# Kernel optimization log

Measured on AMD Instinct MI355X. Metric: run time of the kernel, lower is better.

The kernel has to match this reference:

```python
import jax, jax.numpy as jnp
import numpy as np

B, T, C = 2, 2048, 2048
N_HEAD, KV_HEADS = 16, 4
HEAD_DIM = C // N_HEAD  # 128
EPS = 1e-6


def setup_inputs() -> dict:
    key = jax.random.key(0)
    ks = jax.random.split(key, 3)
    x = jax.random.normal(ks[0], (B, T, C), dtype=jnp.float32)
    qkv_out = (N_HEAD + 2 * KV_HEADS) * HEAD_DIM  # 3072
    w_qkv = jax.random.normal(ks[1], (qkv_out, C), dtype=jnp.float32) * 0.02
    w_proj = jax.random.normal(ks[2], (C, C), dtype=jnp.float32) * 0.02
    q_norm_w = jnp.ones((HEAD_DIM,), dtype=jnp.float32)
    k_norm_w = jnp.ones((HEAD_DIM,), dtype=jnp.float32)
    # RoPE frequencies: theta = 10000^{-2i/d}, angles = pos * theta
    inv_freq = 1.0 / (10000.0 ** (np.arange(0, HEAD_DIM, 2, dtype=np.float32) / HEAD_DIM))
    angles = np.arange(T, dtype=np.float32)[:, None] * inv_freq[None, :]  # [T, 64]
    freqs_cos = jnp.asarray(np.cos(angles), dtype=jnp.float32)
    freqs_sin = jnp.asarray(np.sin(angles), dtype=jnp.float32)
    return {"x": x, "w_qkv": w_qkv, "w_proj": w_proj,
            "q_norm_w": q_norm_w, "k_norm_w": k_norm_w,
            "freqs_cos": freqs_cos, "freqs_sin": freqs_sin}


def _rope(t, cos, sin):
    # t: [B, H, T, D]; interpret last dim as D/2 complex pairs (a, b)
    a = t[..., 0::2]
    b = t[..., 1::2]
    oa = a * cos - b * sin
    ob = a * sin + b * cos
    return jnp.stack([oa, ob], axis=-1).reshape(t.shape)


def _rmsnorm(t, w, eps=EPS):
    rms = jnp.sqrt(jnp.mean(t * t, axis=-1, keepdims=True) + eps)
    return w * (t / rms)


def reference(x, w_qkv, w_proj, q_norm_w, k_norm_w, freqs_cos, freqs_sin):
    b, t, c = x.shape
    hd = HEAD_DIM
    qkv = x @ w_qkv.T  # [B, T, 3072]
    q_size = N_HEAD * hd
    kv_size = KV_HEADS * hd
    q = qkv[..., :q_size].reshape(b, t, N_HEAD, hd).transpose(0, 2, 1, 3)
    k = qkv[..., q_size:q_size + kv_size].reshape(b, t, KV_HEADS, hd).transpose(0, 2, 1, 3)
    v = qkv[..., q_size + kv_size:].reshape(b, t, KV_HEADS, hd).transpose(0, 2, 1, 3)
    # repeat_interleave KV heads to match query heads (GQA)
    rep = N_HEAD // KV_HEADS
    k = jnp.repeat(k, rep, axis=1)
    v = jnp.repeat(v, rep, axis=1)
    # RoPE (applied after repeat, matching the torch code order)
    cos = freqs_cos[:t][None, None, :, :]
    sin = freqs_sin[:t][None, None, :, :]
    q = _rope(q, cos, sin)
    k = _rope(k, cos, sin)
    # QK RMSNorm per head_dim
    q = _rmsnorm(q, q_norm_w)
    k = _rmsnorm(k, k_norm_w)
    # causal SDPA
    scores = jnp.einsum('bhqd,bhkd->bhqk', q, k) / jnp.sqrt(jnp.float32(hd))
    causal = jnp.tril(jnp.ones((t, t), dtype=bool))
    scores = jnp.where(causal[None, None], scores, jnp.finfo(scores.dtype).min)
    att = jax.nn.softmax(scores, axis=-1)
    y = jnp.einsum('bhqk,bhkd->bhqd', att, v)
    y = y.transpose(0, 2, 1, 3).reshape(b, t, c)
    return y @ w_proj.T
```

## Files before the change

### kernel.cpp

```cpp
#include <hip/hip_runtime.h>
#include <hip/hip_bf16.h>

#define B_    2
#define T_    2048
#define C_    2048
#define NH_   16
#define KVH_  4
#define HD_   128
#define QKV_  3072
#define M_    4096

typedef float  floatx4 __attribute__((ext_vector_type(4)));
typedef __bf16 bf16x8  __attribute__((ext_vector_type(8)));
typedef __bf16 bf16x4  __attribute__((ext_vector_type(4)));
typedef __bf16 bf16x2  __attribute__((ext_vector_type(2)));

typedef const __attribute__((address_space(1))) void* gas_t;
typedef __attribute__((address_space(3))) void*       las_t;
__device__ __forceinline__ void gl_lds16(const void* g, void* l) {
  __builtin_amdgcn_global_load_lds((gas_t)g, (las_t)l, 16, 0, 0);
}

__global__ __launch_bounds__(256) void cvt3(const float* __restrict__ s0, __bf16* __restrict__ d0, int n0,
                                            const float* __restrict__ s1, __bf16* __restrict__ d1, int n1,
                                            const float* __restrict__ s2, __bf16* __restrict__ d2, int n2) {
  int i = blockIdx.x * blockDim.x + threadIdx.x;
  const float* s; __bf16* d;
  if (i < n0) { s = s0; d = d0; }
  else {
    i -= n0;
    if (i < n1) { s = s1; d = d1; }
    else { i -= n1; if (i >= n2) return; s = s2; d = d2; }
  }
  float4 f = ((const float4*)s)[i];
  bf16x4 o = { (__bf16)f.x, (__bf16)f.y, (__bf16)f.z, (__bf16)f.w };
  ((bf16x4*)d)[i] = o;
}

template <typename OutT>
__global__ __launch_bounds__(256) void gemm_bt(const __bf16* __restrict__ A,
                                               const __bf16* __restrict__ Bm,
                                               OutT* __restrict__ Cc,
                                               int N, int K) {
  __shared__ __align__(16) __bf16 As[2][128 * 32];
  __shared__ __align__(16) __bf16 Bs[2][128 * 32];
  const int tid  = threadIdx.x;
  const int wid  = tid >> 6, lane = tid & 63, quad = lane >> 4, r16 = lane & 15;
  const int bm   = blockIdx.y * 128, bn = blockIdx.x * 128;
  const int wm   = (wid >> 1) * 64, wn = (wid & 1) * 64;
  const int srow = wid * 16 + (lane >> 2);
  const int scol = (lane & 3) * 8;
  const __bf16* aptr = A  + (size_t)(bm + srow) * K + scol;
  const __bf16* bptr = Bm + (size_t)(bn + srow) * K + scol;
  const size_t rowskip = (size_t)64 * K;

  floatx4 acc[4][4];
  #pragma unroll
  for (int i = 0; i < 4; i++)
    #pragma unroll
    for (int j = 0; j < 4; j++) acc[i][j] = (floatx4){0.f, 0.f, 0.f, 0.f};

  for (int k0 = 0; k0 < K; k0 += 64) {
    #pragma unroll
    for (int hf = 0; hf < 2; hf++) {
      gl_lds16(aptr + k0 + hf * 32,           &As[hf][wid * 512]);
      gl_lds16(aptr + rowskip + k0 + hf * 32, &As[hf][2048 + wid * 512]);
      gl_lds16(bptr + k0 + hf * 32,           &Bs[hf][wid * 512]);
      gl_lds16(bptr + rowskip + k0 + hf * 32, &Bs[hf][2048 + wid * 512]);
    }
    __syncthreads();

    #pragma unroll
    for (int hf = 0; hf < 2; hf++) {
      bf16x8 af[4], bfr[4];
      #pragma unroll
      for (int i = 0; i < 4; i++) af[i]  = *(const bf16x8*)&As[hf][(wm + i * 16 + r16) * 32 + quad * 8];
      #pragma unroll
      for (int j = 0; j < 4; j++) bfr[j] = *(const bf16x8*)&Bs[hf][(wn + j * 16 + r16) * 32 + quad * 8];
      #pragma unroll
      for (int i = 0; i < 4; i++)
        #pragma unroll
        for (int j = 0; j < 4; j++)
          acc[i][j] = __builtin_amdgcn_mfma_f32_16x16x32_bf16(af[i], bfr[j], acc[i][j], 0, 0, 0);
    }
    __syncthreads();
  }

  #pragma unroll
  for (int i = 0; i < 4; i++) {
    #pragma unroll
    for (int reg = 0; reg < 4; reg++) {
      int row = bm + wm + i * 16 + quad * 4 + reg;
      OutT* crow = Cc + (size_t)row * N + bn + wn;
      #pragma unroll
      for (int j = 0; j < 4; j++) crow[j * 16 + r16] = (OutT)acc[i][j][reg];
    }
  }
}

__global__ __launch_bounds__(256) void rope_norm(const __bf16* __restrict__ qkv,
                                                 const float* __restrict__ qw,
                                                 const float* __restrict__ kw,
                                                 const float* __restrict__ fc,
                                                 const float* __restrict__ fs,
                                                 __bf16* __restrict__ qn,
                                                 __bf16* __restrict__ kn) {
  const int tid  = threadIdx.x;
  const int wid  = tid >> 6, lane = tid & 63;
  const int row  = blockIdx.x * 4 + wid;
  const int b    = row >> 11, t = row & (T_ - 1);
  const float cs = fc[t * 64 + lane], sn = fs[t * 64 + lane];
  const __bf16* base = qkv + (size_t)row * QKV_;

  #pragma unroll 2
  for (int h = 0; h < NH_; h++) {
    bf16x2 ab = *(const bf16x2*)(base + h * HD_ + 2 * lane);
    float ax = (float)ab[0], ay = (float)ab[1];
    float oa = ax * cs - ay * sn;
    float ob = ax * sn + ay * cs;
    float ss = oa * oa + ob * ob;
    #pragma unroll
    for (int off = 32; off; off >>= 1) ss += __shfl_xor(ss, off);
    float rinv = rsqrtf(ss * (1.0f / HD_) + 1e-6f);
    bf16x2 o = { (__bf16)(oa * rinv * qw[2 * lane]), (__bf16)(ob * rinv * qw[2 * lane + 1]) };
    *(bf16x2*)&qn[(size_t)((b * NH_ + h) * T_ + t) * HD_ + 2 * lane] = o;
  }
  #pragma unroll 2
  for (int h = 0; h < KVH_; h++) {
    bf16x2 ab = *(const bf16x2*)(base + C_ + h * HD_ + 2 * lane);
    float ax = (float)ab[0], ay = (float)ab[1];
    float oa = ax * cs - ay * sn;
    float ob = ax * sn + ay * cs;
    float ss = oa * oa + ob * ob;
    #pragma unroll
    for (int off = 32; off; off >>= 1) ss += __shfl_xor(ss, off);
    float rinv = rsqrtf(ss * (1.0f / HD_) + 1e-6f);
    bf16x2 o = { (__bf16)(oa * rinv * kw[2 * lane]), (__bf16)(ob * rinv * kw[2 * lane + 1]) };
    *(bf16x2*)&kn[(size_t)((b * KVH_ + h) * T_ + t) * HD_ + 2 * lane] = o;
  }
}

__global__ __launch_bounds__(256) void vtrans(const __bf16* __restrict__ qkv,
                                              __bf16* __restrict__ vT) {
  __shared__ __bf16 L[64 * 68];
  const int tid = threadIdx.x;
  const int t0 = blockIdx.x * 64;
  const int d0 = blockIdx.y * 64;
  const int z  = blockIdx.z;
  const int b  = z >> 2, hk = z & 3;
  const int srcc = C_ + KVH_ * HD_ + hk * HD_ + d0;
  const int rr = tid >> 4, c4 = (tid & 15) * 4;
  #pragma unroll
  for (int i = 0; i < 4; i++) {
    int t = rr + i * 16;
    bf16x4 f = *(const bf16x4*)&qkv[(size_t)(b * T_ + t0 + t) * QKV_ + srcc + c4];
    *(bf16x4*)&L[t * 68 + c4] = f;
  }
  __syncthreads();
  const int dr = tid >> 3, tc8 = (tid & 7) * 8;
  #pragma unroll
  for (int i = 0; i < 2; i++) {
    int d = dr + i * 32;
    bf16x8 ov;
    #pragma unroll
    for (int j = 0; j < 8; j++) ov[j] = L[(tc8 + j) * 68 + d];
    *(bf16x8*)&vT[(size_t)(z * HD_ + d0 + d) * T_ + t0 + tc8] = ov;
  }
}

__device__ __forceinline__ int swz_w(int lane) {
  return ((lane & 3) << 4) | ((lane >> 2) ^ ((lane & 3) << 1));
}
__device__ __forceinline__ int swz_r(int quad, int r16) {
  return (quad << 4) | (r16 ^ (quad << 1));
}

__device__ __forceinline__ void kv_prefetch8(const __bf16* kbase, const __bf16* vbase,
                                             int kt0, int wid, int lane,
                                             bf16x8 kreg[2], bf16x8 vreg[2]) {
  const int r4 = lane >> 2, c8 = (lane & 3) * 8;
  #pragma unroll
  for (int i = 0; i < 2; i++) {
    const int n = wid * 2 + i;
    kreg[i] = *(const bf16x8*)&kbase[(size_t)(kt0 + (n >> 2) * 16 + r4) * HD_ + (n & 3) * 32 + c8];
    vreg[i] = *(const bf16x8*)&vbase[(size_t)((n >> 1) * 16 + r4) * T_ + kt0 + (n & 1) * 32 + c8];
  }
}

__device__ __forceinline__ void kv_commit8(__bf16* Ks, __bf16* Vs, int wid, int lane,
                                           const bf16x8 kreg[2], const bf16x8 vreg[2]) {
  const int slot = swz_w(lane);
  #pragma unroll
  for (int i = 0; i < 2; i++) {
    *(bf16x8*)(Ks + (wid * 2 + i) * 512 + slot * 8) = kreg[i];
    *(bf16x8*)(Vs + (wid * 2 + i) * 512 + slot * 8) = vreg[i];
  }
}

__global__ __launch_bounds__(512, 4) void flash(const __bf16* __restrict__ q,
                                                const __bf16* __restrict__ k,
                                                const __bf16* __restrict__ vT,
                                                __bf16* __restrict__ y) {
  __shared__ __align__(16) __bf16 Ks[64 * 128];
  __shared__ __align__(16) __bf16 Vs[128 * 64];
  __shared__ __align__(16) __bf16 Ps[8][16 * 72];
  const int tid = threadIdx.x;
  const int wid = tid >> 6, lane = tid & 63, quad = lane >> 4, r16 = lane & 15;
  const int x   = blockIdx.x;
  const int p   = (x >> 5) & 7, hl = x & 31;
  const int qt  = (x < 256) ? (15 - p) : p;
  const int b = hl >> 4, h = hl & 15, hk = h >> 2;

  const __bf16* kbase = k  + (size_t)(b * KVH_ + hk) * T_ * HD_;
  const __bf16* vbase = vT + (size_t)(b * KVH_ + hk) * HD_ * T_;
  __bf16* Pw = Ps[wid];
  const float sc = 0.08838834764831845f;
  const float NEG = -__builtin_inff();
  bf16x8 ones;
  #pragma unroll
  for (int i = 0; i < 8; i++) ones[i] = (__bf16)1.0f;

  const int nt = 2 * (qt + 1);
  const int r0 = qt * 128 + wid * 16;

  const __bf16* qrow = q + ((size_t)(b * NH_ + h) * T_ + r0 + r16) * HD_;
  bf16x8 qf[4];
  #pragma unroll
  for (int kb = 0; kb < 4; kb++) qf[kb] = *(const bf16x8*)&qrow[kb * 32 + quad * 8];

  floatx4 o[8], ol = (floatx4){0.f, 0.f, 0.f, 0.f};
  #pragma unroll
  for (int j = 0; j < 8; j++) o[j] = (floatx4){0.f, 0.f, 0.f, 0.f};
  float m_r[4] = {NEG, NEG, NEG, NEG};

  bf16x8 kreg[2], vreg[2];
  kv_prefetch8(kbase, vbase, 0, wid, lane, kreg, vreg);

  #pragma unroll 1
  for (int it = 0; it < nt; ++it) {
    __syncthreads();
    kv_commit8(Ks, Vs, wid, lane, kreg, vreg);
    __syncthreads();
    if (it + 1 < nt) kv_prefetch8(kbase, vbase, (it + 1) * 64, wid, lane, kreg, vreg);

    const int kt0 = it * 64;
    if (kt0 <= r0 + 15) {
      floatx4 s[4];
      #pragma unroll
      for (int cb = 0; cb < 4; cb++) s[cb] = (floatx4){0.f, 0.f, 0.f, 0.f};
      #pragma unroll
      for (int kb = 0; kb < 4; kb++)
        #pragma unroll
        for (int cb = 0; cb < 4; cb++) {
          bf16x8 kf = *(const bf16x8*)&Ks[(cb * 4 + kb) * 512 + swz_r(quad, r16) * 8];
          s[cb] = __builtin_amdgcn_mfma_f32_16x16x32_bf16(qf[kb], kf, s[cb], 0, 0, 0);
        }

      const bool needmask = (kt0 + 63 > r0);
      float alpha[4];
      #pragma unroll
      for (int reg = 0; reg < 4; reg++) {
        const int rowq = r0 + quad * 4 + reg;
        float v0 = s[0][reg] * sc, v1 = s[1][reg] * sc;
        float v2 = s[2][reg] * sc, v3 = s[3][reg] * sc;
        if (needmask) {
          if (kt0 +      r16 > rowq) v0 = NEG;
          if (kt0 + 16 + r16 > rowq) v1 = NEG;
          if (kt0 + 32 + r16 > rowq) v2 = NEG;
          if (kt0 + 48 + r16 > rowq) v3 = NEG;
        }
        float mx = fmaxf(fmaxf(v0, v1), fmaxf(v2, v3));
        #pragma unroll
        for (int off = 8; off; off >>= 1) mx = fmaxf(mx, __shfl_xor(mx, off));
        float mnew = fmaxf(m_r[reg], mx);
        alpha[reg] = __expf(m_r[reg] - mnew);
        m_r[reg] = mnew;
        Pw[(quad * 4 + reg) * 72 +      r16] = (__bf16)__expf(v0 - mnew);
        Pw[(quad * 4 + reg) * 72 + 16 + r16] = (__bf16)__expf(v1 - mnew);
        Pw[(quad * 4 + reg) * 72 + 32 + r16] = (__bf16)__expf(v2 - mnew);
        Pw[(quad * 4 + reg) * 72 + 48 + r16] = (__bf16)__expf(v3 - mnew);
      }
      #pragma unroll
      for (int reg = 0; reg < 4; reg++) {
        ol[reg] *= alpha[reg];
        #pragma unroll
        for (int j = 0; j < 8; j++) o[j][reg] *= alpha[reg];
      }
      __asm__ volatile("" ::: "memory");
      bf16x8 pf0 = *(const bf16x8*)&Pw[r16 * 72 + quad * 8];
      bf16x8 pf1 = *(const bf16x8*)&Pw[r16 * 72 + 32 + quad * 8];
      ol = __builtin_amdgcn_mfma_f32_16x16x32_bf16(pf0, ones, ol, 0, 0, 0);
      ol = __builtin_amdgcn_mfma_f32_16x16x32_bf16(pf1, ones, ol, 0, 0, 0);
      #pragma unroll
      for (int j = 0; j < 8; j++) {
        bf16x8 vf0 = *(const bf16x8*)&Vs[(j * 2 + 0) * 512 + swz_r(quad, r16) * 8];
        bf16x8 vf1 = *(const bf16x8*)&Vs[(j * 2 + 1) * 512 + swz_r(quad, r16) * 8];
        o[j] = __builtin_amdgcn_mfma_f32_16x16x32_bf16(pf0, vf0, o[j], 0, 0, 0);
        o[j] = __builtin_amdgcn_mfma_f32_16x16x32_bf16(pf1, vf1, o[j], 0, 0, 0);
      }
    }
  }

  #pragma unroll
  for (int reg = 0; reg < 4; reg++) {
    int trow = r0 + quad * 4 + reg;
    float inv = 1.0f / ol[reg];
    __bf16* yr = y + ((size_t)(b * T_) + trow) * C_ + h * HD_;
    #pragma unroll
    for (int j = 0; j < 8; j++) yr[j * 16 + r16] = (__bf16)(o[j][reg] * inv);
  }
}

extern "C" void kernel_launch(void* const* d_in, const int* in_sizes, int n_in,
                              void* d_out, int out_size, void* d_ws, size_t ws_size,
                              hipStream_t stream) {
  const float* x     = (const float*)d_in[0];
  const float* wqkv  = (const float*)d_in[1];
  const float* wproj = (const float*)d_in[2];
  const float* qw    = (const float*)d_in[3];
  const float* kw    = (const float*)d_in[4];
  const float* fc    = (const float*)d_in[5];
  const float* fs    = (const float*)d_in[6];
  float* out = (float*)d_out;

  char* w = (char*)d_ws;
  __bf16* xb     = (__bf16*)w; w += (size_t)M_ * C_ * 2;
  __bf16* wqkvb  = (__bf16*)w; w += (size_t)QKV_ * C_ * 2;
  __bf16* wprojb = (__bf16*)w; w += (size_t)C_ * C_ * 2;
  __bf16* qkv    = (__bf16*)w; w += (size_t)M_ * QKV_ * 2;
  __bf16* qn     = (__bf16*)w; w += (size_t)B_ * NH_ * T_ * HD_ * 2;
  __bf16* kn     = (__bf16*)w; w += (size_t)B_ * KVH_ * T_ * HD_ * 2;
  __bf16* vT     = (__bf16*)w; w += (size_t)B_ * KVH_ * T_ * HD_ * 2;
  __bf16* ybf    = (__bf16*)w; w += (size_t)M_ * C_ * 2;

  const int n0 = M_ * C_ / 4, n1 = QKV_ * C_ / 4, n2 = C_ * C_ / 4;
  cvt3<<<(n0 + n1 + n2 + 255) / 256, 256, 0, stream>>>(x, xb, n0, wqkv, wqkvb, n1, wproj, wprojb, n2);

  gemm_bt<__bf16><<<dim3(QKV_ / 128, M_ / 128), 256, 0, stream>>>(xb, wqkvb, qkv, QKV_, C_);
  rope_norm<<<M_ / 4, 256, 0, stream>>>(qkv, qw, kw, fc, fs, qn, kn);
  vtrans<<<dim3(T_ / 64, HD_ / 64, B_ * KVH_), 256, 0, stream>>>(qkv, vT);
  flash<<<dim3(512), 512, 0, stream>>>(qn, kn, vT, ybf);
  gemm_bt<float><<<dim3(C_ / 128, M_ / 128), 256, 0, stream>>>(ybf, wprojb, out, C_, C_);
}
```

Before: 325.9 us.

## Double-buffer K/V tiles in flash attention with lazy softmax rescaling

Converts the single K/V LDS buffer into a ping-pong pair so the next tile is committed while the current one is computed, cutting two barriers per iteration down to one. Adds a lazy online-softmax rescale that only updates the running max and rescales accumulators when any row's max grows by more than a threshold. It also splits the P·V product into two 32-column halves with a smaller P scratch, and raises wave priority around MFMA blocks. This doubles K/V LDS use, which can lower occupancy, and the lazy rescale risks exp overflow or precision loss if the threshold is crossed in bf16.

```diff
diff --git a/kernel.cpp b/kernel.cpp
--- a/kernel.cpp
+++ b/kernel.cpp
@@ -201,9 +201,9 @@
                                                 const __bf16* __restrict__ k,
                                                 const __bf16* __restrict__ vT,
                                                 __bf16* __restrict__ y) {
-  __shared__ __align__(16) __bf16 Ks[64 * 128];
-  __shared__ __align__(16) __bf16 Vs[128 * 64];
-  __shared__ __align__(16) __bf16 Ps[8][16 * 72];
+  __shared__ __align__(16) __bf16 Ks[2][64 * 128];
+  __shared__ __align__(16) __bf16 Vs[2][64 * 128];
+  __shared__ __align__(16) __bf16 Ps[8][16 * 48];
   const int tid = threadIdx.x;
   const int wid = tid >> 6, lane = tid & 63, quad = lane >> 4, r16 = lane & 15;
   const int x   = blockIdx.x;
@@ -235,70 +235,89 @@
 
   bf16x8 kreg[2], vreg[2];
   kv_prefetch8(kbase, vbase, 0, wid, lane, kreg, vreg);
+  kv_commit8(&Ks[0][0], &Vs[0][0], wid, lane, kreg, vreg);
+  if (nt > 1) kv_prefetch8(kbase, vbase, 64, wid, lane, kreg, vreg);
+  __syncthreads();
 
   #pragma unroll 1
   for (int it = 0; it < nt; ++it) {
-    __syncthreads();
-    kv_commit8(Ks, Vs, wid, lane, kreg, vreg);
-    __syncthreads();
-    if (it + 1 < nt) kv_prefetch8(kbase, vbase, (it + 1) * 64, wid, lane, kreg, vreg);
+    if (it + 1 < nt) {
+      kv_commit8(&Ks[(it + 1) & 1][0], &Vs[(it + 1) & 1][0], wid, lane, kreg, vreg);
+      if (it + 2 < nt) kv_prefetch8(kbase, vbase, (it + 2) * 64, wid, lane, kreg, vreg);
+    }
 
     const int kt0 = it * 64;
+    const __bf16* Kb = &Ks[it & 1][0];
+    const __bf16* Vb = &Vs[it & 1][0];
     if (kt0 <= r0 + 15) {
       floatx4 s[4];
       #pragma unroll
       for (int cb = 0; cb < 4; cb++) s[cb] = (floatx4){0.f, 0.f, 0.f, 0.f};
+      __builtin_amdgcn_s_setprio(1);
       #pragma unroll
       for (int kb = 0; kb < 4; kb++)
         #pragma unroll
         for (int cb = 0; cb < 4; cb++) {
-          bf16x8 kf = *(const bf16x8*)&Ks[(cb * 4 + kb) * 512 + swz_r(quad, r16) * 8];
+          bf16x8 kf = *(const bf16x8*)&Kb[(cb * 4 + kb) * 512 + swz_r(quad, r16) * 8];
           s[cb] = __builtin_amdgcn_mfma_f32_16x16x32_bf16(qf[kb], kf, s[cb], 0, 0, 0);
         }
+      __builtin_amdgcn_s_setprio(0);
 
       const bool needmask = (kt0 + 63 > r0);
-      float alpha[4];
       #pragma unroll
       for (int reg = 0; reg < 4; reg++) {
         const int rowq = r0 + quad * 4 + reg;
-        float v0 = s[0][reg] * sc, v1 = s[1][reg] * sc;
-        float v2 = s[2][reg] * sc, v3 = s[3][reg] * sc;
+        s[0][reg] *= sc; s[1][reg] *= sc; s[2][reg] *= sc; s[3][reg] *= sc;
         if (needmask) {
-          if (kt0 +      r16 > rowq) v0 = NEG;
-          if (kt0 + 16 + r16 > rowq) v1 = NEG;
-          if (kt0 + 32 + r16 > rowq) v2 = NEG;
-          if (kt0 + 48 + r16 > rowq) v3 = NEG;
-        }
-        float mx = fmaxf(fmaxf(v0, v1), fmaxf(v2, v3));
-        #pragma unroll
-        for (int off = 8; off; off >>= 1) mx = fmaxf(mx, __shfl_xor(mx, off));
-        float mnew = fmaxf(m_r[reg], mx);
-        alpha[reg] = __expf(m_r[reg] - mnew);
-        m_r[reg] = mnew;
-        Pw[(quad * 4 + reg) * 72 +      r16] = (__bf16)__expf(v0 - mnew);
-        Pw[(quad * 4 + reg) * 72 + 16 + r16] = (__bf16)__expf(v1 - mnew);
-        Pw[(quad * 4 + reg) * 72 + 32 + r16] = (__bf16)__expf(v2 - mnew);
-        Pw[(quad * 4 + reg) * 72 + 48 + r16] = (__bf16)__expf(v3 - mnew);
+          if (kt0 +      r16 > rowq) s[0][reg] = NEG;
+          if (kt0 + 16 + r16 > rowq) s[1][reg] = NEG;
+          if (kt0 + 32 + r16 > rowq) s[2][reg] = NEG;
+          if (kt0 + 48 + r16 > rowq) s[3][reg] = NEG;
+        }
       }
+      float mx[4], mnew[4];
       #pragma unroll
       for (int reg = 0; reg < 4; reg++) {
-        ol[reg] *= alpha[reg];
-        #pragma unroll
-        for (int j = 0; j < 8; j++) o[j][reg] *= alpha[reg];
+        float m0 = fmaxf(fmaxf(s[0][reg], s[1][reg]), fmaxf(s[2][reg], s[3][reg]));
+        #pragma unroll
+        for (int off = 8; off; off >>= 1) m0 = fmaxf(m0, __shfl_xor(m0, off));
+        mx[reg] = m0;
+        mnew[reg] = fmaxf(m_r[reg], m0);
       }
-      __asm__ volatile("" ::: "memory");
-      bf16x8 pf0 = *(const bf16x8*)&Pw[r16 * 72 + quad * 8];
-      bf16x8 pf1 = *(const bf16x8*)&Pw[r16 * 72 + 32 + quad * 8];
-      ol = __builtin_amdgcn_mfma_f32_16x16x32_bf16(pf0, ones, ol, 0, 0, 0);
-      ol = __builtin_amdgcn_mfma_f32_16x16x32_bf16(pf1, ones, ol, 0, 0, 0);
-      #pragma unroll
-      for (int j = 0; j < 8; j++) {
-        bf16x8 vf0 = *(const bf16x8*)&Vs[(j * 2 + 0) * 512 + swz_r(quad, r16) * 8];
-        bf16x8 vf1 = *(const bf16x8*)&Vs[(j * 2 + 1) * 512 + swz_r(quad, r16) * 8];
-        o[j] = __builtin_amdgcn_mfma_f32_16x16x32_bf16(pf0, vf0, o[j], 0, 0, 0);
-        o[j] = __builtin_amdgcn_mfma_f32_16x16x32_bf16(pf1, vf1, o[j], 0, 0, 0);
+      float growth = fmaxf(fmaxf(mx[0] - m_r[0], mx[1] - m_r[1]),
+                           fmaxf(mx[2] - m_r[2], mx[3] - m_r[3]));
+      if (!__all(growth <= 8.0f)) {
+        #pragma unroll
+        for (int reg = 0; reg < 4; reg++) {
+          float a = __expf(m_r[reg] - mnew[reg]);
+          m_r[reg] = mnew[reg];
+          ol[reg] *= a;
+          #pragma unroll
+          for (int j = 0; j < 8; j++) o[j][reg] *= a;
+        }
       }
-    }
+      #pragma unroll
+      for (int c = 0; c < 2; c++) {
+        #pragma unroll
+        for (int reg = 0; reg < 4; reg++) {
+          const int prow = quad * 4 + reg;
+          Pw[prow * 48 +      r16] = (__bf16)__expf(s[2 * c    ][reg] - m_r[reg]);
+          Pw[prow * 48 + 16 + r16] = (__bf16)__expf(s[2 * c + 1][reg] - m_r[reg]);
+        }
+        __asm__ volatile("" ::: "memory");
+        bf16x8 pf = *(const bf16x8*)&Pw[r16 * 48 + quad * 8];
+        __builtin_amdgcn_s_setprio(1);
+        ol = __builtin_amdgcn_mfma_f32_16x16x32_bf16(pf, ones, ol, 0, 0, 0);
+        #pragma unroll
+        for (int j = 0; j < 8; j++) {
+          bf16x8 vf = *(const bf16x8*)&Vb[(j * 2 + c) * 512 + swz_r(quad, r16) * 8];
+          o[j] = __builtin_amdgcn_mfma_f32_16x16x32_bf16(pf, vf, o[j], 0, 0, 0);
+        }
+        __builtin_amdgcn_s_setprio(0);
+        __asm__ volatile("" ::: "memory");
+      }
+    }
+    __syncthreads();
   }
 
   #pragma unroll
```

Result: no change. 322.5 us (-1.1%).
